# Kernel optimization log

Measured on AMD Instinct MI355X. Metric: run time of the kernel, lower is better.

Reference implementation:

```python
import jax, jax.numpy as jnp
import numpy as np

E = 1024  # embed_dim
H = 16    # num_heads
D = E // H  # head_dim


def setup_inputs() -> dict:
    key = jax.random.key(0)
    ks = jax.random.split(key, 9)
    s = 0.02
    return {
        "hidden_state": jax.random.normal(ks[0], (4, 1024, E), jnp.float32),
        "Wq": jax.random.normal(ks[1], (H, D, E), jnp.float32) * s,
        "bq": jax.random.normal(ks[2], (H, D), jnp.float32) * s,
        "Wk": jax.random.normal(ks[3], (H, D, E), jnp.float32) * s,
        "bk": jax.random.normal(ks[4], (H, D), jnp.float32) * s,
        "Wv": jax.random.normal(ks[5], (H, D, E), jnp.float32) * s,
        "bv": jax.random.normal(ks[6], (H, D), jnp.float32) * s,
        "Wo": jax.random.normal(ks[7], (E, E), jnp.float32) * s,
        "bo": jax.random.normal(ks[8], (E,), jnp.float32) * s,
    }


def _mha(x, Wq, bq, Wk, bk, Wv, bv, Wo, bo):
    # Per-head linear projections (torch Linear: y = x W^T + b), batched over heads.
    q = jnp.einsum("bse,hde->bhsd", x, Wq) + bq[None, :, None, :]
    k = jnp.einsum("bse,hde->bhsd", x, Wk) + bk[None, :, None, :]
    v = jnp.einsum("bse,hde->bhsd", x, Wv) + bv[None, :, None, :]
    scores = jnp.einsum("bhsd,bhtd->bhst", q, k) / jnp.sqrt(jnp.asarray(D, x.dtype))
    w = jax.nn.softmax(scores, axis=-1)  # F.softmax default -> last dim
    o = jnp.einsum("bhst,bhtd->bhsd", w, v)
    # concat heads along last dim: [B,S,H*D] in head order (matches torch.cat)
    B, _, S, _ = o.shape
    o = jnp.transpose(o, (0, 2, 1, 3)).reshape(B, S, H * D)
    return o @ Wo.T + bo


def reference(hidden_state, Wq, bq, Wk, bk, Wv, bv, Wo, bo):
    return _mha(hidden_state, Wq, bq, Wk, bk, Wv, bv, Wo, bo)
```

## Files before the change

kernel.cpp:

```cpp
#include <hip/hip_runtime.h>
#include <hip/hip_bf16.h>
#include <stdint.h>

#define E_DIM 1024
#define H_NUM 16
#define D_DIM 64
#define B_NUM 4
#define S_LEN 1024

typedef __attribute__((ext_vector_type(8))) short bf16x8;
typedef __attribute__((ext_vector_type(4))) short bf16x4;
typedef __attribute__((ext_vector_type(4))) float f32x4;

#define SOFTMAX_C2 0.18033688011112042f

__device__ inline ushort f2b(float x) {
    __hip_bfloat16 h = __float2bfloat16(x);
    return *(ushort*)&h;
}
__device__ inline float b2f(ushort u) {
    __hip_bfloat16 h = *(__hip_bfloat16*)&u;
    return __bfloat162float(h);
}
__device__ inline uint pk2(float a, float b) {
    __hip_bfloat162 h = __float22bfloat162_rn(make_float2(a, b));
    return *(uint*)&h;
}
__device__ inline float fexp2(float x) { return __builtin_amdgcn_exp2f(x); }

__device__ inline void gld16(const ushort* g, ushort* l) {
    __builtin_amdgcn_global_load_lds((const __attribute__((address_space(1))) void*)g,
                                     (__attribute__((address_space(3))) void*)l, 16, 0, 0);
}

__global__ __launch_bounds__(256)
void convert_all(const float* __restrict__ X,  const float* __restrict__ Wq,
                 const float* __restrict__ Wk, const float* __restrict__ Wv,
                 const float* __restrict__ Wo,
                 ushort* __restrict__ Xb, ushort* __restrict__ Wcat,
                 ushort* __restrict__ Wob)
{
    const int bid = blockIdx.x;
    const float* src; ushort* dst; size_t off;
    if (bid < 4096)      { src = X;  dst = Xb;   off = (size_t)bid * 1024; }
    else if (bid < 5120) { src = Wq; dst = Wcat;              off = (size_t)(bid - 4096) * 1024; }
    else if (bid < 6144) { src = Wk; dst = Wcat + (1u << 20); off = (size_t)(bid - 5120) * 1024; }
    else if (bid < 7168) { src = Wv; dst = Wcat + (2u << 20); off = (size_t)(bid - 6144) * 1024; }
    else                 { src = Wo; dst = Wob;               off = (size_t)(bid - 7168) * 1024; }
    const size_t i = off + (size_t)threadIdx.x * 4;
    float4 v = *(const float4*)&src[i];
    ushort4 o;
    o.x = f2b(v.x); o.y = f2b(v.y); o.z = f2b(v.z); o.w = f2b(v.w);
    *(ushort4*)&dst[i] = o;
}

__global__ __launch_bounds__(256, 2)
void gemm_qkv(const ushort* __restrict__ A, const ushort* __restrict__ Bw,
              const float* __restrict__ b0, const float* __restrict__ b1,
              const float* __restrict__ b2,
              ushort* __restrict__ Qb, ushort* __restrict__ Kb,
              ushort* __restrict__ Vt_g, int K)
{
    __shared__ __align__(16) ushort SM[32768];
    ushort* As = SM;
    ushort* Bs = SM + 16384;

    const int tid  = threadIdx.x;
    const int wave = tid >> 6;
    const int lane = tid & 63;
    const int quad = lane >> 4;
    const int l16  = lane & 15;
    const int wm   = wave & 1;
    const int wn   = wave >> 1;
    const int m0   = blockIdx.x * 128;
    const int n0   = blockIdx.y * 128;

    f32x4 acc[4][4] = {};

    auto stageA = [&](int buf, int k0) {
#pragma unroll
        for (int i = 0; i < 4; ++i) {
            const int e   = i * 256 + tid;
            const int row = e >> 3;
            const int gc8 = ((e & 7) ^ (row & 7)) * 8;
            gld16(&A[(size_t)(m0 + row) * K + k0 + gc8], &As[buf * 8192 + e * 8]);
        }
    };
    auto stageB = [&](int buf, int k0) {
#pragma unroll
        for (int i = 0; i < 4; ++i) {
            const int e   = i * 256 + tid;
            const int row = e >> 3;
            const int gc8 = ((e & 7) ^ (row & 7)) * 8;
            gld16(&Bw[(size_t)(n0 + row) * K + k0 + gc8], &Bs[buf * 8192 + e * 8]);
        }
    };

    stageA(0, 0); stageB(0, 0);
    __syncthreads();

    const int nk = K >> 6;
    const int xa = (l16 & 7) * 8;
    for (int ki = 0; ki < nk; ++ki) {
        const int cur = ki & 1;
        if (ki + 1 < nk) { stageA(cur ^ 1, (ki + 1) << 6); stageB(cur ^ 1, (ki + 1) << 6); }

#pragma unroll
        for (int ks = 0; ks < 2; ++ks) {
            const int lc = (ks * 32 + quad * 8) ^ xa;
            bf16x8 af[4], bf[4];
#pragma unroll
            for (int mi = 0; mi < 4; ++mi)
                af[mi] = *(const bf16x8*)&As[cur * 8192 + (wm * 64 + mi * 16 + l16) * 64 + lc];
#pragma unroll
            for (int ni = 0; ni < 4; ++ni)
                bf[ni] = *(const bf16x8*)&Bs[cur * 8192 + (wn * 64 + ni * 16 + l16) * 64 + lc];
#pragma unroll
            for (int mi = 0; mi < 4; ++mi)
#pragma unroll
                for (int ni = 0; ni < 4; ++ni)
                    acc[mi][ni] = __builtin_amdgcn_mfma_f32_16x16x32_bf16(af[mi], bf[ni], acc[mi][ni], 0, 0, 0);
        }
        __syncthreads();
    }

    const int seg   = n0 >> 10;
    const int cbase = n0 & 1023;
    const float* bp = (seg == 0) ? b0 : (seg == 1) ? b1 : b2;
    const float scl = (seg == 0) ? SOFTMAX_C2 : 1.0f;

    if (seg < 2) {
        ushort* T = SM;
#pragma unroll
        for (int ni = 0; ni < 4; ++ni) {
            const int nloc = wn * 64 + ni * 16 + l16;
            const float bv = bp[cbase + nloc];
#pragma unroll
            for (int mi = 0; mi < 4; ++mi)
#pragma unroll
                for (int r = 0; r < 4; ++r)
                    T[(wm * 64 + mi * 16 + quad * 4 + r) * 136 + nloc] =
                        f2b((acc[mi][ni][r] + bv) * scl);
        }
        __syncthreads();
        ushort* dst = (seg == 0) ? Qb : Kb;
        const int row = tid >> 1, half = tid & 1;
        const ushort* s = &T[row * 136 + half * 64];
        ushort* d = &dst[(size_t)(m0 + row) * 1024 + cbase + half * 64];
#pragma unroll
        for (int j = 0; j < 8; ++j)
            *(uint4*)(d + j * 8) = *(const uint4*)(s + j * 8);
    } else {
        ushort* Tt = SM;
        const int b  = m0 >> 10, sbase = m0 & 1023;
#pragma unroll
        for (int ni = 0; ni < 4; ++ni) {
            const int nloc = wn * 64 + ni * 16 + l16;
            const float bv = bp[cbase + nloc];
#pragma unroll
            for (int mi = 0; mi < 4; ++mi) {
                const int mloc = wm * 64 + mi * 16 + quad * 4;
                ushort4 pk;
                pk.x = f2b(acc[mi][ni][0] + bv);
                pk.y = f2b(acc[mi][ni][1] + bv);
                pk.z = f2b(acc[mi][ni][2] + bv);
                pk.w = f2b(acc[mi][ni][3] + bv);
                *(ushort4*)&Tt[nloc * 136 + mloc] = pk;
            }
        }
        __syncthreads();
        const int nrow = tid >> 1, half = tid & 1;
        const int hh   = (cbase >> 6) + (nrow >> 6);
        const int drow = nrow & 63;
        const ushort* s = &Tt[nrow * 136 + half * 64];
        ushort* d = &Vt_g[(((size_t)(b * 16 + hh)) * 64 + drow) * 1024 + sbase + half * 64];
#pragma unroll
        for (int j = 0; j < 8; ++j)
            *(uint4*)(d + j * 8) = *(const uint4*)(s + j * 8);
    }
}

__global__ __launch_bounds__(128, 4)
void attention12(const ushort* __restrict__ Qg, const ushort* __restrict__ Kg,
                 const ushort* __restrict__ Vg, ushort* __restrict__ Anorm)
{
    __shared__ __align__(16) ushort SM[9216];

    const int tid  = threadIdx.x;
    const int w    = tid >> 6;
    const int lane = tid & 63;
    const int quad = lane >> 4;
    const int l16  = lane & 15;

    const int gid = blockIdx.x;
    const int qt  = (gid >> 3) & 31;
    const int bh  = (gid & 7) | ((gid >> 8) << 3);
    const int b   = bh >> 4;
    const int h   = bh & 15;
    const size_t tbase = ((size_t)b * S_LEN) * E_DIM + (size_t)h * D_DIM;
    const size_t vbase = (size_t)bh * D_DIM * S_LEN;

    const ushort* qrow = Qg + tbase + (size_t)(qt * 32 + w * 16 + l16) * E_DIM + quad * 8;
    bf16x8 qf[2];
    qf[0] = *(const bf16x8*)qrow;
    qf[1] = *(const bf16x8*)(qrow + 32);

    const int krow = tid >> 3, kslot = tid & 7;
    const int vr   = tid >> 2, vc = (tid & 3) * 8;

    const ushort* kptr = Kg + tbase + (size_t)krow * E_DIM + ((kslot ^ (krow & 7)) * 8);
    const ushort* vptr = Vg + vbase + (size_t)vr * S_LEN + vc;

    gld16(kptr,               &SM[tid * 8]);
    gld16(kptr + 16 * E_DIM,  &SM[(128 + tid) * 8]);
    {
        uint4 v0 = *(const uint4*)vptr;
        uint4 v1 = *(const uint4*)(vptr + 32 * S_LEN);
        *(uint4*)&SM[4096 + vr * 36 + vc]        = v0;
        *(uint4*)&SM[4096 + (vr + 32) * 36 + vc] = v1;
    }
    __syncthreads();

    float lq = 0.0f;
    f32x4 oacc[4] = {};
    const int xk = (l16 & 7);

    for (int kt = 0; kt < 32; ++kt) {
        const int cur = kt & 1;

        uint4 vpre0, vpre1;
        if (kt < 31) {
            kptr += 32 * E_DIM;
            gld16(kptr,              &SM[(cur ^ 1) * 2048 + tid * 8]);
            gld16(kptr + 16 * E_DIM, &SM[(cur ^ 1) * 2048 + (128 + tid) * 8]);
            vptr += 32;
            vpre0 = *(const uint4*)vptr;
            vpre1 = *(const uint4*)(vptr + 32 * S_LEN);
        }

        f32x4 sacc[2] = {};
        __builtin_amdgcn_s_setprio(1);
#pragma unroll
        for (int mt = 0; mt < 2; ++mt)
#pragma unroll
            for (int ks = 0; ks < 2; ++ks) {
                bf16x8 kf = *(const bf16x8*)&SM[cur * 2048 + (mt * 16 + l16) * 64 +
                                                (((ks * 4 + quad) ^ xk) * 8)];
                sacc[mt] = __builtin_amdgcn_mfma_f32_16x16x32_bf16(kf, qf[ks], sacc[mt], 0, 0, 0);
            }
        __builtin_amdgcn_s_setprio(0);

        bf16x4 pf[2];
        float rs = 0.0f;
#pragma unroll
        for (int mt = 0; mt < 2; ++mt) {
            float p0 = fexp2(sacc[mt][0]);
            float p1 = fexp2(sacc[mt][1]);
            float p2 = fexp2(sacc[mt][2]);
            float p3 = fexp2(sacc[mt][3]);
            rs += (p0 + p1) + (p2 + p3);
            union { uint uu[2]; bf16x4 v; } pk;
            pk.uu[0] = pk2(p0, p1);
            pk.uu[1] = pk2(p2, p3);
            pf[mt] = pk.v;
        }
        lq += rs;

        __builtin_amdgcn_s_setprio(1);
#pragma unroll
        for (int nb = 0; nb < 4; ++nb)
#pragma unroll
            for (int kb = 0; kb < 2; ++kb) {
                bf16x4 vf = *(const bf16x4*)&SM[4096 + cur * 2304 +
                                                (nb * 16 + l16) * 36 + kb * 16 + quad * 4];
                oacc[nb] = __builtin_amdgcn_mfma_f32_16x16x16bf16_1k(pf[kb], vf, oacc[nb], 0, 0, 0);
            }
        __builtin_amdgcn_s_setprio(0);

        if (kt < 31) {
            *(uint4*)&SM[4096 + (cur ^ 1) * 2304 + vr * 36 + vc]        = vpre0;
            *(uint4*)&SM[4096 + (cur ^ 1) * 2304 + (vr + 32) * 36 + vc] = vpre1;
        }
        __syncthreads();
    }

    lq += __shfl_xor(lq, 16);
    lq += __shfl_xor(lq, 32);

    float linv[4];
#pragma unroll
    for (int r = 0; r < 4; ++r)
        linv[r] = __builtin_amdgcn_rcpf(__shfl(lq, quad * 4 + r));

    ushort* T = SM;
#pragma unroll
    for (int nb = 0; nb < 4; ++nb)
#pragma unroll
        for (int r = 0; r < 4; ++r)
            T[(w * 16 + quad * 4 + r) * 72 + nb * 16 + l16] = f2b(oacc[nb][r] * linv[r]);
    __syncthreads();
    {
        const int row = tid >> 2, c16 = (tid & 3) * 16;
        const ushort* s = &T[row * 72 + c16];
        ushort* d = &Anorm[(size_t)(b * 1024 + qt * 32 + row) * 1024 + h * 64 + c16];
        *(uint4*)(d)     = *(const uint4*)(s);
        *(uint4*)(d + 8) = *(const uint4*)(s + 8);
    }
}

__global__ __launch_bounds__(256, 2)
void gemm_out(const ushort* __restrict__ A, const ushort* __restrict__ Bw,
              const float* __restrict__ bias, float* __restrict__ Cout)
{
    __shared__ __align__(16) ushort SM[24576];
    ushort* As = SM;
    ushort* Bs = SM + 16384;

    const int tid  = threadIdx.x;
    const int wave = tid >> 6;
    const int lane = tid & 63;
    const int quad = lane >> 4;
    const int l16  = lane & 15;
    const int wm   = wave & 1;
    const int wn   = wave >> 1;
    const int m0   = blockIdx.x * 128;
    const int n0   = blockIdx.y * 64;

    f32x4 acc[4][2] = {};

    auto stageA = [&](int buf, int k0) {
#pragma unroll
        for (int i = 0; i < 4; ++i) {
            const int e   = i * 256 + tid;
            const int row = e >> 3;
            const int gc8 = ((e & 7) ^ (row & 7)) * 8;
            gld16(&A[(size_t)(m0 + row) * 1024 + k0 + gc8], &As[buf * 8192 + e * 8]);
        }
    };
    auto stageB = [&](int buf, int k0) {
#pragma unroll
        for (int i = 0; i < 2; ++i) {
            const int e   = i * 256 + tid;
            const int row = e >> 3;
            const int gc8 = ((e & 7) ^ (row & 7)) * 8;
            gld16(&Bw[(size_t)(n0 + row) * 1024 + k0 + gc8], &Bs[buf * 4096 + e * 8]);
        }
    };

    stageA(0, 0); stageB(0, 0);
    __syncthreads();

    const int xa = (l16 & 7) * 8;
    for (int ki = 0; ki < 16; ++ki) {
        const int cur = ki & 1;
        if (ki + 1 < 16) { stageA(cur ^ 1, (ki + 1) << 6); stageB(cur ^ 1, (ki + 1) << 6); }

#pragma unroll
        for (int ks = 0; ks < 2; ++ks) {
            const int lc = (ks * 32 + quad * 8) ^ xa;
            bf16x8 af[4], bf[2];
#pragma unroll
            for (int mi = 0; mi < 4; ++mi)
                af[mi] = *(const bf16x8*)&As[cur * 8192 + (wm * 64 + mi * 16 + l16) * 64 + lc];
#pragma unroll
            for (int ni = 0; ni < 2; ++ni)
                bf[ni] = *(const bf16x8*)&Bs[cur * 4096 + (wn * 32 + ni * 16 + l16) * 64 + lc];
#pragma unroll
            for (int mi = 0; mi < 4; ++mi)
#pragma unroll
                for (int ni = 0; ni < 2; ++ni)
                    acc[mi][ni] = __builtin_amdgcn_mfma_f32_16x16x32_bf16(af[mi], bf[ni], acc[mi][ni], 0, 0, 0);
        }
        __syncthreads();
    }

    float* Tf = (float*)SM;
#pragma unroll
    for (int ni = 0; ni < 2; ++ni) {
        const int nloc = wn * 32 + ni * 16 + l16;
        const float bv = bias[n0 + nloc];
#pragma unroll
        for (int mi = 0; mi < 4; ++mi)
#pragma unroll
            for (int r = 0; r < 4; ++r)
                Tf[(wm * 64 + mi * 16 + quad * 4 + r) * 68 + nloc] = acc[mi][ni][r] + bv;
    }
    __syncthreads();
    {
        const int row = tid >> 1, half = tid & 1;
        const float* s = &Tf[row * 68 + half * 32];
        float* d = &Cout[(size_t)(m0 + row) * 1024 + n0 + half * 32];
#pragma unroll
        for (int j = 0; j < 8; ++j)
            *(float4*)(d + j * 4) = *(const float4*)(s + j * 4);
    }
}

extern "C" void kernel_launch(void* const* d_in, const int* in_sizes, int n_in,
                              void* d_out, int out_size, void* d_ws, size_t ws_size,
                              hipStream_t stream)
{
    (void)in_sizes; (void)n_in; (void)out_size; (void)ws_size;

    const float* X  = (const float*)d_in[0];
    const float* Wq = (const float*)d_in[1];
    const float* bq = (const float*)d_in[2];
    const float* Wk = (const float*)d_in[3];
    const float* bk = (const float*)d_in[4];
    const float* Wv = (const float*)d_in[5];
    const float* bv = (const float*)d_in[6];
    const float* Wo = (const float*)d_in[7];
    const float* bo = (const float*)d_in[8];

    const size_t MEG = 1u << 20;
    ushort* ws    = (ushort*)d_ws;
    ushort* Xb    = ws;
    ushort* Wcat  = ws + 4 * MEG;
    ushort* Wob   = ws + 7 * MEG;
    ushort* Qb    = ws + 8 * MEG;
    ushort* Kb    = ws + 12 * MEG;
    ushort* Vtg   = ws + 16 * MEG;
    ushort* Anorm = ws + 20 * MEG;

    dim3 blk(256);

    convert_all<<<8192, blk, 0, stream>>>(X, Wq, Wk, Wv, Wo, Xb, Wcat, Wob);

    gemm_qkv<<<dim3(32, 24), blk, 0, stream>>>(Xb, Wcat, bq, bk, bv,
                                               Qb, Kb, Vtg, E_DIM);

    attention12<<<2048, dim3(128), 0, stream>>>(Qb, Kb, Vtg, Anorm);

    gemm_out<<<dim3(32, 16), blk, 0, stream>>>(Anorm, Wob, bo, (float*)d_out);
}
```

Baseline: 177.1 us.

## Load K/V fragments directly into registers, drop LDS staging and barriers

The attention kernel no longer stages K and V tiles through shared memory with per-iteration barriers. Each wave now loads its MFMA K and V fragments straight from global memory into registers, double-buffered across two tiles. Blocks grow to 256 threads covering 64 query rows, which halves the grid. The aim is to remove LDS round-trips and __syncthreads stalls, at the cost of four waves redundantly fetching the same K/V data through cache with less coalesced access patterns.

```diff
diff --git a/kernel.cpp b/kernel.cpp
--- a/kernel.cpp
+++ b/kernel.cpp
@@ -180,11 +180,11 @@
     }
 }
 
-__global__ __launch_bounds__(128, 4)
-void attention12(const ushort* __restrict__ Qg, const ushort* __restrict__ Kg,
+__global__ __launch_bounds__(256, 4)
+void attention13(const ushort* __restrict__ Qg, const ushort* __restrict__ Kg,
                  const ushort* __restrict__ Vg, ushort* __restrict__ Anorm)
 {
-    __shared__ __align__(16) ushort SM[9216];
+    __shared__ __align__(16) ushort SM[4608];
 
     const int tid  = threadIdx.x;
     const int w    = tid >> 6;
@@ -193,61 +193,47 @@
     const int l16  = lane & 15;
 
     const int gid = blockIdx.x;
-    const int qt  = (gid >> 3) & 31;
-    const int bh  = (gid & 7) | ((gid >> 8) << 3);
+    const int qt  = (gid >> 3) & 15;
+    const int bh  = (gid & 7) | ((gid >> 7) << 3);
     const int b   = bh >> 4;
     const int h   = bh & 15;
     const size_t tbase = ((size_t)b * S_LEN) * E_DIM + (size_t)h * D_DIM;
     const size_t vbase = (size_t)bh * D_DIM * S_LEN;
 
-    const ushort* qrow = Qg + tbase + (size_t)(qt * 32 + w * 16 + l16) * E_DIM + quad * 8;
+    const ushort* qrow = Qg + tbase + (size_t)(qt * 64 + w * 16 + l16) * E_DIM + quad * 8;
     bf16x8 qf[2];
     qf[0] = *(const bf16x8*)qrow;
     qf[1] = *(const bf16x8*)(qrow + 32);
 
-    const int krow = tid >> 3, kslot = tid & 7;
-    const int vr   = tid >> 2, vc = (tid & 3) * 8;
-
-    const ushort* kptr = Kg + tbase + (size_t)krow * E_DIM + ((kslot ^ (krow & 7)) * 8);
-    const ushort* vptr = Vg + vbase + (size_t)vr * S_LEN + vc;
-
-    gld16(kptr,               &SM[tid * 8]);
-    gld16(kptr + 16 * E_DIM,  &SM[(128 + tid) * 8]);
-    {
-        uint4 v0 = *(const uint4*)vptr;
-        uint4 v1 = *(const uint4*)(vptr + 32 * S_LEN);
-        *(uint4*)&SM[4096 + vr * 36 + vc]        = v0;
-        *(uint4*)&SM[4096 + (vr + 32) * 36 + vc] = v1;
-    }
-    __syncthreads();
+    const ushort* kfb = Kg + tbase + (size_t)l16 * E_DIM + quad * 8;
+    const ushort* vfb = Vg + vbase + (size_t)l16 * E_DIM + quad * 4;
+
+    auto loadK = [&](int kt, bf16x8 (&kf)[2][2]) {
+#pragma unroll
+        for (int mt = 0; mt < 2; ++mt)
+#pragma unroll
+            for (int ks = 0; ks < 2; ++ks)
+                kf[mt][ks] = *(const bf16x8*)&kfb[(size_t)(kt * 32 + mt * 16) * E_DIM + ks * 32];
+    };
+    auto loadV = [&](int kt, bf16x4 (&vf)[4][2]) {
+#pragma unroll
+        for (int nb = 0; nb < 4; ++nb)
+#pragma unroll
+            for (int kb = 0; kb < 2; ++kb)
+                vf[nb][kb] = *(const bf16x4*)&vfb[(size_t)(nb * 16) * S_LEN + kt * 32 + kb * 16];
+    };
 
     float lq = 0.0f;
     f32x4 oacc[4] = {};
-    const int xk = (l16 & 7);
-
-    for (int kt = 0; kt < 32; ++kt) {
-        const int cur = kt & 1;
-
-        uint4 vpre0, vpre1;
-        if (kt < 31) {
-            kptr += 32 * E_DIM;
-            gld16(kptr,              &SM[(cur ^ 1) * 2048 + tid * 8]);
-            gld16(kptr + 16 * E_DIM, &SM[(cur ^ 1) * 2048 + (128 + tid) * 8]);
-            vptr += 32;
-            vpre0 = *(const uint4*)vptr;
-            vpre1 = *(const uint4*)(vptr + 32 * S_LEN);
-        }
-
+
+    auto tile = [&](const bf16x8 (&kf)[2][2], const bf16x4 (&vf)[4][2]) {
         f32x4 sacc[2] = {};
         __builtin_amdgcn_s_setprio(1);
 #pragma unroll
         for (int mt = 0; mt < 2; ++mt)
 #pragma unroll
-            for (int ks = 0; ks < 2; ++ks) {
-                bf16x8 kf = *(const bf16x8*)&SM[cur * 2048 + (mt * 16 + l16) * 64 +
-                                                (((ks * 4 + quad) ^ xk) * 8)];
-                sacc[mt] = __builtin_amdgcn_mfma_f32_16x16x32_bf16(kf, qf[ks], sacc[mt], 0, 0, 0);
-            }
+            for (int ks = 0; ks < 2; ++ks)
+                sacc[mt] = __builtin_amdgcn_mfma_f32_16x16x32_bf16(kf[mt][ks], qf[ks], sacc[mt], 0, 0, 0);
         __builtin_amdgcn_s_setprio(0);
 
         bf16x4 pf[2];
@@ -270,18 +256,20 @@
 #pragma unroll
         for (int nb = 0; nb < 4; ++nb)
 #pragma unroll
-            for (int kb = 0; kb < 2; ++kb) {
-                bf16x4 vf = *(const bf16x4*)&SM[4096 + cur * 2304 +
-                                                (nb * 16 + l16) * 36 + kb * 16 + quad * 4];
-                oacc[nb] = __builtin_amdgcn_mfma_f32_16x16x16bf16_1k(pf[kb], vf, oacc[nb], 0, 0, 0);
-            }
+            for (int kb = 0; kb < 2; ++kb)
+                oacc[nb] = __builtin_amdgcn_mfma_f32_16x16x16bf16_1k(pf[kb], vf[nb][kb], oacc[nb], 0, 0, 0);
         __builtin_amdgcn_s_setprio(0);
-
-        if (kt < 31) {
-            *(uint4*)&SM[4096 + (cur ^ 1) * 2304 + vr * 36 + vc]        = vpre0;
-            *(uint4*)&SM[4096 + (cur ^ 1) * 2304 + (vr + 32) * 36 + vc] = vpre1;
-        }
-        __syncthreads();
+    };
+
+    bf16x8 kfA[2][2], kfB[2][2];
+    bf16x4 vfA[4][2], vfB[4][2];
+    loadK(0, kfA); loadV(0, vfA);
+
+    for (int kt = 0; kt < 32; kt += 2) {
+        loadK(kt + 1, kfB); loadV(kt + 1, vfB);
+        tile(kfA, vfA);
+        if (kt + 2 < 32) { loadK(kt + 2, kfA); loadV(kt + 2, vfA); }
+        tile(kfB, vfB);
     }
 
     lq += __shfl_xor(lq, 16);
@@ -302,7 +290,7 @@
     {
         const int row = tid >> 2, c16 = (tid & 3) * 16;
         const ushort* s = &T[row * 72 + c16];
-        ushort* d = &Anorm[(size_t)(b * 1024 + qt * 32 + row) * 1024 + h * 64 + c16];
+        ushort* d = &Anorm[(size_t)(b * 1024 + qt * 64 + row) * 1024 + h * 64 + c16];
         *(uint4*)(d)     = *(const uint4*)(s);
         *(uint4*)(d + 8) = *(const uint4*)(s + 8);
     }
@@ -429,7 +417,7 @@
     gemm_qkv<<<dim3(32, 24), blk, 0, stream>>>(Xb, Wcat, bq, bk, bv,
                                                Qb, Kb, Vtg, E_DIM);
 
-    attention12<<<2048, dim3(128), 0, stream>>>(Qb, Kb, Vtg, Anorm);
+    attention13<<<1024, blk, 0, stream>>>(Qb, Kb, Vtg, Anorm);
 
     gemm_out<<<dim3(32, 16), blk, 0, stream>>>(Anorm, Wob, bo, (float*)d_out);
 }
```

Result: slower. 314.1 us (+77.3%).

## Enlarge attention blocks to 64 queries and remap GEMM blocks per XCD

Applied to the files above, without the earlier changes.

The attention kernel goes from 128-thread blocks covering 32 query rows to 256-thread blocks covering 64 query rows. Each K/V tile staged in shared memory is now reused by twice as many queries, the grid is halved, and the s_setprio hints are removed. The QKV and output GEMMs switch to a 1D grid whose block index is swizzled so that consecutive M tiles land on the same XCD, aiming for better L2 reuse of shared operand rows. The trade-offs are fewer attention blocks in flight, a different occupancy target, and the loss of the wave-priority scheduling hints.

```diff
diff --git a/kernel.cpp b/kernel.cpp
--- a/kernel.cpp
+++ b/kernel.cpp
@@ -72,8 +72,12 @@
     const int l16  = lane & 15;
     const int wm   = wave & 1;
     const int wn   = wave >> 1;
-    const int m0   = blockIdx.x * 128;
-    const int n0   = blockIdx.y * 128;
+
+    const int bid = blockIdx.x;
+    const int xcd = bid & 7;
+    const int j   = bid >> 3;
+    const int m0  = (xcd * 4 + (j & 3)) * 128;
+    const int n0  = (j >> 2) * 128;
 
     f32x4 acc[4][4] = {};
 
@@ -148,8 +152,8 @@
         const ushort* s = &T[row * 136 + half * 64];
         ushort* d = &dst[(size_t)(m0 + row) * 1024 + cbase + half * 64];
 #pragma unroll
-        for (int j = 0; j < 8; ++j)
-            *(uint4*)(d + j * 8) = *(const uint4*)(s + j * 8);
+        for (int j2 = 0; j2 < 8; ++j2)
+            *(uint4*)(d + j2 * 8) = *(const uint4*)(s + j2 * 8);
     } else {
         ushort* Tt = SM;
         const int b  = m0 >> 10, sbase = m0 & 1023;
@@ -175,13 +179,13 @@
         const ushort* s = &Tt[nrow * 136 + half * 64];
         ushort* d = &Vt_g[(((size_t)(b * 16 + hh)) * 64 + drow) * 1024 + sbase + half * 64];
 #pragma unroll
-        for (int j = 0; j < 8; ++j)
-            *(uint4*)(d + j * 8) = *(const uint4*)(s + j * 8);
-    }
-}
-
-__global__ __launch_bounds__(128, 4)
-void attention12(const ushort* __restrict__ Qg, const ushort* __restrict__ Kg,
+        for (int j2 = 0; j2 < 8; ++j2)
+            *(uint4*)(d + j2 * 8) = *(const uint4*)(s + j2 * 8);
+    }
+}
+
+__global__ __launch_bounds__(256, 8)
+void attention11(const ushort* __restrict__ Qg, const ushort* __restrict__ Kg,
                  const ushort* __restrict__ Vg, ushort* __restrict__ Anorm)
 {
     __shared__ __align__(16) ushort SM[9216];
@@ -193,14 +197,14 @@
     const int l16  = lane & 15;
 
     const int gid = blockIdx.x;
-    const int qt  = (gid >> 3) & 31;
-    const int bh  = (gid & 7) | ((gid >> 8) << 3);
+    const int qt  = (gid >> 3) & 15;
+    const int bh  = (gid & 7) | ((gid >> 7) << 3);
     const int b   = bh >> 4;
     const int h   = bh & 15;
     const size_t tbase = ((size_t)b * S_LEN) * E_DIM + (size_t)h * D_DIM;
     const size_t vbase = (size_t)bh * D_DIM * S_LEN;
 
-    const ushort* qrow = Qg + tbase + (size_t)(qt * 32 + w * 16 + l16) * E_DIM + quad * 8;
+    const ushort* qrow = Qg + tbase + (size_t)(qt * 64 + w * 16 + l16) * E_DIM + quad * 8;
     bf16x8 qf[2];
     qf[0] = *(const bf16x8*)qrow;
     qf[1] = *(const bf16x8*)(qrow + 32);
@@ -211,13 +215,10 @@
     const ushort* kptr = Kg + tbase + (size_t)krow * E_DIM + ((kslot ^ (krow & 7)) * 8);
     const ushort* vptr = Vg + vbase + (size_t)vr * S_LEN + vc;
 
-    gld16(kptr,               &SM[tid * 8]);
-    gld16(kptr + 16 * E_DIM,  &SM[(128 + tid) * 8]);
+    gld16(kptr, &SM[tid * 8]);
     {
         uint4 v0 = *(const uint4*)vptr;
-        uint4 v1 = *(const uint4*)(vptr + 32 * S_LEN);
-        *(uint4*)&SM[4096 + vr * 36 + vc]        = v0;
-        *(uint4*)&SM[4096 + (vr + 32) * 36 + vc] = v1;
+        *(uint4*)&SM[4096 + vr * 36 + vc] = v0;
     }
     __syncthreads();
 
@@ -228,18 +229,15 @@
     for (int kt = 0; kt < 32; ++kt) {
         const int cur = kt & 1;
 
-        uint4 vpre0, vpre1;
+        uint4 vpre;
         if (kt < 31) {
             kptr += 32 * E_DIM;
-            gld16(kptr,              &SM[(cur ^ 1) * 2048 + tid * 8]);
-            gld16(kptr + 16 * E_DIM, &SM[(cur ^ 1) * 2048 + (128 + tid) * 8]);
+            gld16(kptr, &SM[(cur ^ 1) * 2048 + tid * 8]);
             vptr += 32;
-            vpre0 = *(const uint4*)vptr;
-            vpre1 = *(const uint4*)(vptr + 32 * S_LEN);
+            vpre = *(const uint4*)vptr;
         }
 
         f32x4 sacc[2] = {};
-        __builtin_amdgcn_s_setprio(1);
 #pragma unroll
         for (int mt = 0; mt < 2; ++mt)
 #pragma unroll
@@ -248,7 +246,6 @@
                                                 (((ks * 4 + quad) ^ xk) * 8)];
                 sacc[mt] = __builtin_amdgcn_mfma_f32_16x16x32_bf16(kf, qf[ks], sacc[mt], 0, 0, 0);
             }
-        __builtin_amdgcn_s_setprio(0);
 
         bf16x4 pf[2];
         float rs = 0.0f;
@@ -266,7 +263,6 @@
         }
         lq += rs;
 
-        __builtin_amdgcn_s_setprio(1);
 #pragma unroll
         for (int nb = 0; nb < 4; ++nb)
 #pragma unroll
@@ -275,12 +271,9 @@
                                                 (nb * 16 + l16) * 36 + kb * 16 + quad * 4];
                 oacc[nb] = __builtin_amdgcn_mfma_f32_16x16x16bf16_1k(pf[kb], vf, oacc[nb], 0, 0, 0);
             }
-        __builtin_amdgcn_s_setprio(0);
-
-        if (kt < 31) {
-            *(uint4*)&SM[4096 + (cur ^ 1) * 2304 + vr * 36 + vc]        = vpre0;
-            *(uint4*)&SM[4096 + (cur ^ 1) * 2304 + (vr + 32) * 36 + vc] = vpre1;
-        }
+
+        if (kt < 31)
+            *(uint4*)&SM[4096 + (cur ^ 1) * 2304 + vr * 36 + vc] = vpre;
         __syncthreads();
     }
 
@@ -302,7 +295,7 @@
     {
         const int row = tid >> 2, c16 = (tid & 3) * 16;
         const ushort* s = &T[row * 72 + c16];
-        ushort* d = &Anorm[(size_t)(b * 1024 + qt * 32 + row) * 1024 + h * 64 + c16];
+        ushort* d = &Anorm[(size_t)(b * 1024 + qt * 64 + row) * 1024 + h * 64 + c16];
         *(uint4*)(d)     = *(const uint4*)(s);
         *(uint4*)(d + 8) = *(const uint4*)(s + 8);
     }
@@ -323,8 +316,12 @@
     const int l16  = lane & 15;
     const int wm   = wave & 1;
     const int wn   = wave >> 1;
-    const int m0   = blockIdx.x * 128;
-    const int n0   = blockIdx.y * 64;
+
+    const int bid = blockIdx.x;
+    const int xcd = bid & 7;
+    const int j   = bid >> 3;
+    const int m0  = (xcd * 4 + (j & 3)) * 128;
+    const int n0  = (j >> 2) * 64;
 
     f32x4 acc[4][2] = {};
 
@@ -391,8 +388,8 @@
         const float* s = &Tf[row * 68 + half * 32];
         float* d = &Cout[(size_t)(m0 + row) * 1024 + n0 + half * 32];
 #pragma unroll
-        for (int j = 0; j < 8; ++j)
-            *(float4*)(d + j * 4) = *(const float4*)(s + j * 4);
+        for (int j2 = 0; j2 < 8; ++j2)
+            *(float4*)(d + j2 * 4) = *(const float4*)(s + j2 * 4);
     }
 }
 
@@ -426,10 +423,10 @@
 
     convert_all<<<8192, blk, 0, stream>>>(X, Wq, Wk, Wv, Wo, Xb, Wcat, Wob);
 
-    gemm_qkv<<<dim3(32, 24), blk, 0, stream>>>(Xb, Wcat, bq, bk, bv,
-                                               Qb, Kb, Vtg, E_DIM);
-
-    attention12<<<2048, dim3(128), 0, stream>>>(Qb, Kb, Vtg, Anorm);
-
-    gemm_out<<<dim3(32, 16), blk, 0, stream>>>(Anorm, Wob, bo, (float*)d_out);
-}
+    gemm_qkv<<<768, blk, 0, stream>>>(Xb, Wcat, bq, bk, bv,
+                                      Qb, Kb, Vtg, E_DIM);
+
+    attention11<<<1024, blk, 0, stream>>>(Qb, Kb, Vtg, Anorm);
+
+    gemm_out<<<512, blk, 0, stream>>>(Anorm, Wob, bo, (float*)d_out);
+}
```

New measurement: 174.3 us. Within noise of the previous version (-1.6%).
